# Performance work log

Measured on AMD Instinct MI355X. Metric: run time of the kernel, lower is better.

## Reference

```python
import jax, jax.numpy as jnp
import numpy as np

HEADS = 16
D_MODEL = 1024
D_K = D_MODEL // HEADS
B, S = 2, 2048
NEG = -1000000000.0


def setup_inputs() -> dict:
    key = jax.random.key(0)
    ks = jax.random.split(key, 8)
    q = jax.random.normal(ks[0], (B, S, D_MODEL), dtype=jnp.float32)
    k = jax.random.normal(ks[1], (B, S, D_MODEL), dtype=jnp.float32)
    v = jax.random.normal(ks[2], (B, S, D_MODEL), dtype=jnp.float32)
    mask = jax.random.randint(ks[3], (B, 1, S, S), 0, 2) > 0  # True = masked
    scale = 1.0 / np.sqrt(D_MODEL)
    Wq = jax.random.normal(ks[4], (D_MODEL, D_MODEL), dtype=jnp.float32) * scale
    Wk = jax.random.normal(ks[5], (D_MODEL, D_MODEL), dtype=jnp.float32) * scale
    Wv = jax.random.normal(ks[6], (D_MODEL, D_MODEL), dtype=jnp.float32) * scale
    Wo = jax.random.normal(ks[7], (D_MODEL, D_MODEL), dtype=jnp.float32) * scale
    return {"q": q, "k": k, "v": v, "mask": mask,
            "Wq": Wq, "Wk": Wk, "Wv": Wv, "Wo": Wo}


def reference(q, k, v, mask, Wq, Wk, Wv, Wo):
    b, s, _ = q.shape
    # torch Linear: x @ W.T ; reshape to [B, H, S, d_k]
    def proj(x, W):
        return (x @ W.T).reshape(b, -1, HEADS, D_K).transpose(0, 2, 1, 3)
    qh, kh, vh = proj(q, Wq), proj(k, Wk), proj(v, Wv)
    # scaled dot-product attention; scale uses d_k (key.shape[-1] after reshape)
    att = jnp.einsum('bhqd,bhkd->bhqk', qh, kh) / jnp.sqrt(jnp.float32(D_K))
    att = jnp.where(mask, NEG, att)
    att = jax.nn.softmax(att, axis=-1)
    out = jnp.einsum('bhqk,bhkd->bhqd', att, vh)  # [B,H,S,d_k]
    out = out.transpose(0, 2, 1, 3).reshape(b, -1, D_MODEL)
    return out @ Wo.T  # dropout is identity at inference
```

## Files before the change

kernel.cpp:

```cpp
#include <hip/hip_runtime.h>

typedef unsigned short u16;
typedef unsigned int   u32;
typedef unsigned char  u8;
typedef unsigned long long u64;
typedef __attribute__((ext_vector_type(8))) short bf16x8;
typedef __attribute__((ext_vector_type(4))) float f32x4;
typedef __attribute__((ext_vector_type(16))) float f32x16;

__device__ __forceinline__ u16 f2b(float f) {
  union { float f; u32 u; } v; v.f = f;
  u32 u = v.u;
  return (u16)((u + 0x7fffu + ((u >> 16) & 1u)) >> 16);
}
__device__ __forceinline__ float b2f(u16 x) {
  union { u32 u; float f; } v; v.u = ((u32)x) << 16; return v.f;
}
__device__ __forceinline__ u32 pk2(u16 lo, u16 hi) { return (u32)lo | ((u32)hi << 16); }

__device__ __forceinline__ float fexp2(float x) { return __builtin_amdgcn_exp2f(x); }

__device__ __forceinline__ u32 cvtpk(float lo, float hi) {
  u32 r;
  asm("v_cvt_pk_bf16_f32 %0, %1, %2" : "=v"(r) : "v"(lo), "v"(hi));
  return r;
}

__device__ __forceinline__ void swap32(u32& a, u32& b) {
  asm("v_permlane32_swap_b32 %0, %1" : "+v"(a), "+v"(b));
}

__device__ __forceinline__ void glds16(const u16* g, u16* l) {
  __builtin_amdgcn_global_load_lds((const __attribute__((address_space(1))) void*)g,
                                   (__attribute__((address_space(3))) void*)l, 16, 0, 0);
}

__global__ __launch_bounds__(256) void mask_detect(const u8* __restrict__ raw,
                                                   int* __restrict__ flag) {
  int i = blockIdx.x * 256 + threadIdx.x;
  uint4 x = ((const uint4*)raw)[i];
  u32 o = x.x | x.y | x.z | x.w;
  u64 b1 = __ballot((o & 0x0000ff00u) != 0);
  u64 b2 = __ballot((o & 0xffff0000u) != 0);
  if ((threadIdx.x & 63) == 0) {
    if (b1) atomicOr(&flag[0], 1);
    if (b2) atomicOr(&flag[1], 1);
  }
}

__global__ __launch_bounds__(256) void mask_bits(const u8* __restrict__ raw,
                                                 u64* __restrict__ out,
                                                 const int* __restrict__ flag) {
  int f = flag[0] ? 2 : (flag[1] ? 1 : 0);
  int t = blockIdx.x * 256 + threadIdx.x;
  u8 byte;
  if (f == 2) {
    u64 x = ((const u64*)raw)[t];
    u64 nz = x | (x >> 4); nz |= nz >> 2; nz |= nz >> 1;
    nz &= 0x0101010101010101ull;
    byte = (u8)((nz * 0x0102040810204080ull) >> 56);
  } else if (f == 0) {
    const int* ip = (const int*)raw + t * 8;
    int4 a = *(const int4*)ip, b = *(const int4*)(ip + 4);
    byte = (u8)((a.x != 0) | ((a.y != 0) << 1) | ((a.z != 0) << 2) | ((a.w != 0) << 3) |
                ((b.x != 0) << 4) | ((b.y != 0) << 5) | ((b.z != 0) << 6) | ((b.w != 0) << 7));
  } else {
    const float* fp = (const float*)raw + t * 8;
    float4 a = *(const float4*)fp, b = *(const float4*)(fp + 4);
    byte = (u8)((a.x != 0.f) | ((a.y != 0.f) << 1) | ((a.z != 0.f) << 2) | ((a.w != 0.f) << 3) |
                ((b.x != 0.f) << 4) | ((b.y != 0.f) << 5) | ((b.z != 0.f) << 6) | ((b.w != 0.f) << 7));
  }
  ((u8*)out)[t] = byte;
}

__global__ __launch_bounds__(256) void conv_all(
    const float* __restrict__ W0, const float* __restrict__ W1,
    const float* __restrict__ W2, const float* __restrict__ W3,
    const float* __restrict__ A0, const float* __restrict__ A1,
    const float* __restrict__ A2,
    u16* __restrict__ o0, u16* __restrict__ o1, u16* __restrict__ o2,
    u16* __restrict__ o3, u16* __restrict__ o4, u16* __restrict__ o5,
    u16* __restrict__ o6) {
  int gid = blockIdx.x * 256 + threadIdx.x;
  const float* src; u16* dst; int off;
  if (gid < 524288) {
    int wz = gid >> 17; off = (gid & 131071) * 8;
    src = wz == 0 ? W0 : wz == 1 ? W1 : wz == 2 ? W2 : W3;
    dst = wz == 0 ? o0 : wz == 1 ? o1 : wz == 2 ? o2 : o3;
  } else {
    int g2 = gid - 524288;
    int az = g2 >> 19; off = (g2 & 524287) * 8;
    src = az == 0 ? A0 : az == 1 ? A1 : A2;
    dst = az == 0 ? o4 : az == 1 ? o5 : o6;
  }
  float4 a = *(const float4*)(src + off), b2 = *(const float4*)(src + off + 4);
  uint4 t;
  t.x = pk2(f2b(a.x), f2b(a.y));   t.y = pk2(f2b(a.z), f2b(a.w));
  t.z = pk2(f2b(b2.x), f2b(b2.y)); t.w = pk2(f2b(b2.z), f2b(b2.w));
  *(uint4*)(dst + off) = t;
}

template<int CF32, int DBUF>
__device__ __forceinline__ void gemm_body(
    const u16* __restrict__ Av, const u16* __restrict__ Bv, void* __restrict__ Cv,
    int N, int K, int m0, int n0, float cscale, u16* As, u16* Bs) {
  const int tid = threadIdx.x;
  const int lane = tid & 63, w = tid >> 6;
  const int lr = lane & 15, lg = lane >> 4;
  const int wm = (w >> 1) * 64, wn = (w & 1) * 64;
  const int srow = lane >> 3;
  const int selem = (((lane & 7) ^ srow) << 3);
  const int rsw = (lr & 7) << 3;

  f32x4 acc[4][4];
#pragma unroll
  for (int mi = 0; mi < 4; ++mi)
#pragma unroll
    for (int ni = 0; ni < 4; ++ni)
      acc[mi][ni] = (f32x4){0.f, 0.f, 0.f, 0.f};

#define GLDS2(k0_, LA, LB)                                                     \
  do {                                                                         \
    _Pragma("unroll")                                                          \
    for (int r_ = 0; r_ < 4; ++r_) {                                           \
      const int c_ = w * 4 + r_;                                               \
      const int row_ = c_ * 8 + srow;                                          \
      glds16(Av + (size_t)(m0 + row_) * K + (k0_) + selem, (LA) + c_ * 512);   \
      glds16(Bv + (size_t)(n0 + row_) * K + (k0_) + selem, (LB) + c_ * 512);   \
    }                                                                          \
  } while (0)

#define FRAG_MFMA(bufA, bufB)                                                  \
  do {                                                                         \
    bf16x8 af[4][2], bfv[4][2];                                                \
    _Pragma("unroll")                                                          \
    for (int mi = 0; mi < 4; ++mi)                                             \
      _Pragma("unroll")                                                        \
      for (int kk = 0; kk < 2; ++kk)                                           \
        af[mi][kk] = *(bf16x8*)&(bufA)[(wm + mi * 16 + lr) * 64 + ((kk * 32 + lg * 8) ^ rsw)]; \
    _Pragma("unroll")                                                          \
    for (int ni = 0; ni < 4; ++ni)                                             \
      _Pragma("unroll")                                                        \
      for (int kk = 0; kk < 2; ++kk)                                           \
        bfv[ni][kk] = *(bf16x8*)&(bufB)[(wn + ni * 16 + lr) * 64 + ((kk * 32 + lg * 8) ^ rsw)]; \
    __builtin_amdgcn_s_setprio(1);                                             \
    _Pragma("unroll")                                                          \
    for (int mi = 0; mi < 4; ++mi)                                             \
      _Pragma("unroll")                                                        \
      for (int ni = 0; ni < 4; ++ni)                                           \
        _Pragma("unroll")                                                      \
        for (int kk = 0; kk < 2; ++kk)                                         \
          acc[mi][ni] = __builtin_amdgcn_mfma_f32_16x16x32_bf16(               \
              af[mi][kk], bfv[ni][kk], acc[mi][ni], 0, 0, 0);                  \
    __builtin_amdgcn_s_setprio(0);                                             \
  } while (0)

  if (DBUF) {
    GLDS2(0, As, Bs);
    __syncthreads();
    int cur = 0;
    for (int k0 = 0; k0 < K; k0 += 64) {
      if (k0 + 64 < K) GLDS2(k0 + 64, As + (cur ^ 1) * 8192, Bs + (cur ^ 1) * 8192);
      FRAG_MFMA(As + cur * 8192, Bs + cur * 8192);
      __syncthreads();
      cur ^= 1;
    }
  } else {
    for (int k0 = 0; k0 < K; k0 += 64) {
      __syncthreads();
      GLDS2(k0, As, Bs);
      __syncthreads();
      FRAG_MFMA(As, Bs);
    }
  }
#undef GLDS2
#undef FRAG_MFMA
#pragma unroll
  for (int mi = 0; mi < 4; ++mi)
#pragma unroll
    for (int ni = 0; ni < 4; ++ni)
#pragma unroll
      for (int r = 0; r < 4; ++r) {
        int m = m0 + wm + mi * 16 + lg * 4 + r;
        int n = n0 + wn + ni * 16 + lr;
        float vv = acc[mi][ni][r] * cscale;
        if (CF32) ((float*)Cv)[(size_t)m * N + n] = vv;
        else      ((u16*)Cv)[(size_t)m * N + n] = f2b(vv);
      }
}

__global__ __launch_bounds__(256) void gemm_qkv(
    const u16* __restrict__ qb, const u16* __restrict__ kb, const u16* __restrict__ vb,
    const u16* __restrict__ Wqb, const u16* __restrict__ Wkb, const u16* __restrict__ Wvb,
    u16* __restrict__ Qb, u16* __restrict__ Kb, u16* __restrict__ VTb, float qscale) {
  __shared__ __align__(16) u16 As[8192];
  __shared__ __align__(16) u16 Bs[8192];
  const int z = blockIdx.z;
  const int xcd = blockIdx.x & 7, r = blockIdx.x >> 3;
  const int pblk = xcd * 4 + (r & 3);
  const int oblk = r >> 2;
  if (z < 2) {
    const u16* act = z ? kb : qb;
    const u16* Wb = z ? Wkb : Wqb;
    u16* Cb = z ? Kb : Qb;
    gemm_body<0, 0>(act, Wb, Cb, 1024, 1024, pblk * 128, oblk * 128,
                    z ? 1.0f : qscale, As, Bs);
  } else {
    gemm_body<0, 0>(Wvb, vb, VTb, 4096, 1024, oblk * 128, pblk * 128, 1.0f, As, Bs);
  }
}

__device__ __forceinline__ void gemm64_body(
    const u16* __restrict__ Av, const u16* __restrict__ Bv, float* __restrict__ Cv,
    int N, int K, int m0, int n0, u16* As, u16* Bs) {
  const int tid = threadIdx.x;
  const int lane = tid & 63, w = tid >> 6;
  const int lr = lane & 15, lg = lane >> 4;
  const int wm = w * 32;
  const int srow = lane >> 3;
  const int selem = (((lane & 7) ^ srow) << 3);
  const int rsw = (lr & 7) << 3;

  f32x4 acc[2][4];
#pragma unroll
  for (int mi = 0; mi < 2; ++mi)
#pragma unroll
    for (int ni = 0; ni < 4; ++ni)
      acc[mi][ni] = (f32x4){0.f, 0.f, 0.f, 0.f};

  for (int k0 = 0; k0 < K; k0 += 64) {
    __syncthreads();
#pragma unroll
    for (int r_ = 0; r_ < 4; ++r_) {
      const int c_ = w * 4 + r_;
      const int row_ = c_ * 8 + srow;
      glds16(Av + (size_t)(m0 + row_) * K + k0 + selem, As + c_ * 512);
    }
#pragma unroll
    for (int r_ = 0; r_ < 2; ++r_) {
      const int c_ = w * 2 + r_;
      const int row_ = c_ * 8 + srow;
      glds16(Bv + (size_t)(n0 + row_) * K + k0 + selem, Bs + c_ * 512);
    }
    __syncthreads();
    bf16x8 af[2][2], bfv[4][2];
#pragma unroll
    for (int mi = 0; mi < 2; ++mi)
#pragma unroll
      for (int kk = 0; kk < 2; ++kk)
        af[mi][kk] = *(bf16x8*)&As[(wm + mi * 16 + lr) * 64 + ((kk * 32 + lg * 8) ^ rsw)];
#pragma unroll
    for (int ni = 0; ni < 4; ++ni)
#pragma unroll
      for (int kk = 0; kk < 2; ++kk)
        bfv[ni][kk] = *(bf16x8*)&Bs[(ni * 16 + lr) * 64 + ((kk * 32 + lg * 8) ^ rsw)];
    __builtin_amdgcn_s_setprio(1);
#pragma unroll
    for (int mi = 0; mi < 2; ++mi)
#pragma unroll
      for (int ni = 0; ni < 4; ++ni)
#pragma unroll
        for (int kk = 0; kk < 2; ++kk)
          acc[mi][ni] = __builtin_amdgcn_mfma_f32_16x16x32_bf16(
              af[mi][kk], bfv[ni][kk], acc[mi][ni], 0, 0, 0);
    __builtin_amdgcn_s_setprio(0);
  }
#pragma unroll
  for (int mi = 0; mi < 2; ++mi)
#pragma unroll
    for (int ni = 0; ni < 4; ++ni)
#pragma unroll
      for (int r = 0; r < 4; ++r) {
        int m = m0 + wm + mi * 16 + lg * 4 + r;
        int n = n0 + ni * 16 + lr;
        Cv[(size_t)m * N + n] = acc[mi][ni][r];
      }
}

__global__ __launch_bounds__(256) void gemm_o(
    const u16* __restrict__ Ob, const u16* __restrict__ Wob, float* __restrict__ C) {
  __shared__ __align__(16) u16 As[128 * 64];
  __shared__ __align__(16) u16 Bs[64 * 64];
  const int xcd = blockIdx.x & 7, r = blockIdx.x >> 3;
  const int mblk = xcd * 4 + (r & 3), nblk = r >> 2;
  gemm64_body(Ob, Wob, C, 1024, 1024, mblk * 128, nblk * 64, As, Bs);
}

__global__ __launch_bounds__(256, 4) void flash13(const u16* __restrict__ Q,
                                                  const u16* __restrict__ K,
                                                  const u16* __restrict__ VT,
                                                  const u64* __restrict__ mpk,
                                                  u16* __restrict__ O0,
                                                  u16* __restrict__ O1,
                                                  u16* __restrict__ O2,
                                                  float* __restrict__ Lp) {
  __shared__ __align__(16) u16 Ks[4096];
  __shared__ __align__(16) u16 Vs[4096];
  const int tid = threadIdx.x, lane = tid & 63, w = tid >> 6;
  const int c = lane & 31, h = lane >> 5;
  const int bid = blockIdx.x;
  const int xcd = bid & 7, idx = bid >> 3;
  const int gl = idx >> 4, qblk = idx & 15;
  const int group = xcd * 12 + gl;
  const int split = group % 3;
  const int hb = group / 3;
  const int head = hb & 15, b = hb >> 4;
  const int qw = qblk * 128 + w * 32;
  const int kt0 = (split * 32) / 3;
  const int ktn = ((split + 1) * 32) / 3;
  const int nt = ktn - kt0;
  const size_t kbase = (size_t)b * 2048 * 1024 + (size_t)head * 64;
  const size_t vbase = (size_t)head * 64 * 4096 + (size_t)b * 2048;
  const int srow = lane >> 3;
  const int selem = (((lane & 7) ^ srow) << 3);
  const int rswc = (c & 7) << 3;

  bf16x8 qf[4];
#pragma unroll
  for (int kd = 0; kd < 4; ++kd)
    qf[kd] = *(const bf16x8*)&Q[kbase + (size_t)(qw + c) * 1024 + 16 * kd + 8 * h];

  union { u32 u[4]; bf16x8 v; } ones;
#pragma unroll
  for (int i = 0; i < 4; ++i) ones.u[i] = 0x3f803f80u;

  f32x16 accO0, accO1, accL;
#pragma unroll
  for (int i = 0; i < 16; ++i) { accO0[i] = 0.f; accO1[i] = 0.f; accL[i] = 0.f; }

  const u64* mrp = mpk + ((size_t)b * 2048 + qw + c) * 32;

  for (int t = 0; t < nt; ++t) {
    __syncthreads();
    {
      const int k0_ = (kt0 + t) * 64;
#pragma unroll
      for (int r_ = 0; r_ < 2; ++r_) {
        const int c_ = w * 2 + r_;
        const int row_ = c_ * 8 + srow;
        glds16(K + kbase + (size_t)(k0_ + row_) * 1024 + selem, &Ks[c_ * 512]);
      }
#pragma unroll
      for (int r_ = 0; r_ < 2; ++r_) {
        const int c_ = w * 2 + r_;
        const int row_ = c_ * 8 + srow;
        glds16(VT + vbase + (size_t)row_ * 4096 + k0_ + selem, &Vs[c_ * 512]);
      }
    }
    const u64 mb = mrp[kt0 + t];
    __syncthreads();
    f32x16 s0, s1;
#pragma unroll
    for (int i = 0; i < 16; ++i) { s0[i] = 0.f; s1[i] = 0.f; }
    __builtin_amdgcn_s_setprio(1);
#pragma unroll
    for (int kd = 0; kd < 4; ++kd) {
      bf16x8 kf0 = *(bf16x8*)&Ks[c * 64 + ((16 * kd + 8 * h) ^ rswc)];
      s0 = __builtin_amdgcn_mfma_f32_32x32x16_bf16(kf0, qf[kd], s0, 0, 0, 0);
      bf16x8 kf1 = *(bf16x8*)&Ks[(32 + c) * 64 + ((16 * kd + 8 * h) ^ rswc)];
      s1 = __builtin_amdgcn_mfma_f32_32x32x16_bf16(kf1, qf[kd], s1, 0, 0, 0);
    }
    __builtin_amdgcn_s_setprio(0);
    u32 pw[2][4][2];
#pragma unroll
    for (int kb = 0; kb < 2; ++kb) {
      const u32 m32 = (u32)(mb >> (32 * kb + 4 * h));
      float pp[16];
#pragma unroll
      for (int g = 0; g < 4; ++g)
#pragma unroll
        for (int r = 0; r < 4; ++r) {
          float e = fexp2(kb == 0 ? s0[4 * g + r] : s1[4 * g + r]);
          pp[4 * g + r] = ((m32 >> (8 * g + r)) & 1) ? 0.0f : e;
        }
#pragma unroll
      for (int g = 0; g < 4; ++g)
#pragma unroll
        for (int hh = 0; hh < 2; ++hh)
          pw[kb][g][hh] = cvtpk(pp[4 * g + 2 * hh], pp[4 * g + 2 * hh + 1]);
    }
    __builtin_amdgcn_s_setprio(1);
#pragma unroll
    for (int kb = 0; kb < 2; ++kb)
#pragma unroll
      for (int s = 0; s < 2; ++s) {
        u32 w0 = pw[kb][2 * s][0], w2 = pw[kb][2 * s + 1][0];
        swap32(w0, w2);
        u32 w1 = pw[kb][2 * s][1], w3 = pw[kb][2 * s + 1][1];
        swap32(w1, w3);
        union { u32 u[4]; bf16x8 v; } af;
        af.u[0] = w0; af.u[1] = w1; af.u[2] = w2; af.u[3] = w3;
        const int ksg = kb * 2 + s;
        bf16x8 vf0 = *(bf16x8*)&Vs[c * 64 + ((16 * ksg + 8 * h) ^ rswc)];
        accO0 = __builtin_amdgcn_mfma_f32_32x32x16_bf16(af.v, vf0, accO0, 0, 0, 0);
        bf16x8 vf1 = *(bf16x8*)&Vs[(32 + c) * 64 + ((16 * ksg + 8 * h) ^ rswc)];
        accO1 = __builtin_amdgcn_mfma_f32_32x32x16_bf16(af.v, vf1, accO1, 0, 0, 0);
        accL  = __builtin_amdgcn_mfma_f32_32x32x16_bf16(af.v, ones.v, accL, 0, 0, 0);
      }
    __builtin_amdgcn_s_setprio(0);
  }
  u16* Op = split == 0 ? O0 : split == 1 ? O1 : O2;
  const size_t obase = (size_t)b * 2048 + qw;
#pragma unroll
  for (int g = 0; g < 4; ++g)
#pragma unroll
    for (int r = 0; r < 4; ++r) {
      const int qrow = r + 8 * g + 4 * h;
      const size_t row = obase + qrow;
      const size_t base = row * 1024 + (size_t)head * 64 + c;
      Op[base]      = f2b(accO0[4 * g + r]);
      Op[base + 32] = f2b(accO1[4 * g + r]);
      if (c == 0) Lp[(size_t)split * 65536 + row * 16 + head] = accL[4 * g + r];
    }
}

__global__ __launch_bounds__(256) void combine(const u16* __restrict__ O0,
                                               const u16* __restrict__ O1,
                                               const u16* __restrict__ O2,
                                               const float* __restrict__ Lp,
                                               u16* __restrict__ Ob) {
  int gid = blockIdx.x * 256 + threadIdx.x;
  int row = gid >> 7, chb = (gid & 127) * 8;
  int head = chb >> 6;
  float l = Lp[(size_t)row * 16 + head] + Lp[65536 + (size_t)row * 16 + head] +
            Lp[131072 + (size_t)row * 16 + head];
  float inv = 1.0f / l;
  size_t off = (size_t)row * 1024 + chb;
  union { uint4 q; u16 s[8]; } a, b, c2, o;
  a.q  = *(const uint4*)(O0 + off);
  b.q  = *(const uint4*)(O1 + off);
  c2.q = *(const uint4*)(O2 + off);
#pragma unroll
  for (int j = 0; j < 8; ++j)
    o.s[j] = f2b((b2f(a.s[j]) + b2f(b.s[j]) + b2f(c2.s[j])) * inv);
  *(uint4*)(Ob + off) = o.q;
}

extern "C" void kernel_launch(void* const* d_in, const int* in_sizes, int n_in,
                              void* d_out, int out_size, void* d_ws, size_t ws_size,
                              hipStream_t stream) {
  const float* q    = (const float*)d_in[0];
  const float* k    = (const float*)d_in[1];
  const float* v    = (const float*)d_in[2];
  const u8*    mask = (const u8*)d_in[3];
  const float* Wq   = (const float*)d_in[4];
  const float* Wk   = (const float*)d_in[5];
  const float* Wv   = (const float*)d_in[6];
  const float* Wo   = (const float*)d_in[7];

  u8* ws = (u8*)d_ws;
  int* flag = (int*)ws;
  u64* mpk  = (u64*)(ws + 256);
  u16* Wqb  = (u16*)(ws + 256 + (1u << 20));
  u16* Wkb  = Wqb + (1 << 20);
  u16* Wvb  = Wkb + (1 << 20);
  u16* Wob  = Wvb + (1 << 20);
  const size_t NE = (size_t)4096 * 1024;
  u16* vb   = Wob + (1 << 20);
  u16* O2   = vb;
  u16* Qb   = vb + NE;
  u16* Kb   = Qb + NE;
  u16* VTb  = Kb + NE;
  u16* qb   = (u16*)d_out;
  u16* kb   = qb + NE;
  u16* O0   = qb;
  u16* O1   = kb;
  float* Lp = (float*)Wqb;
  u16* Ob   = Qb;

  const float LOG2E = 1.4426950408889634f;

  hipMemsetAsync(flag, 0, 8, stream);
  mask_detect<<<32, 256, 0, stream>>>(mask, flag);
  mask_bits<<<4096, 256, 0, stream>>>(mask, mpk, flag);
  conv_all<<<8192, 256, 0, stream>>>(Wq, Wk, Wv, Wo, q, k, v,
                                     Wqb, Wkb, Wvb, Wob, qb, kb, vb);

  gemm_qkv<<<dim3(256, 1, 3), 256, 0, stream>>>(
      qb, kb, vb, Wqb, Wkb, Wvb, Qb, Kb, VTb, 0.125f * LOG2E);

  flash13<<<1536, 256, 0, stream>>>(Qb, Kb, VTb, mpk, O0, O1, O2, Lp);
  combine<<<2048, 256, 0, stream>>>(O0, O1, O2, Lp, Ob);

  gemm_o<<<512, 256, 0, stream>>>(Ob, Wob, (float*)d_out);
}
```

Before: 141.3 us.

## Register-prefetch next K/V tile in flash kernel instead of direct global-to-LDS loads

Swaps the direct global-to-LDS loads (glds16) for loads into registers that fetch the next K/V tile and mask word one iteration ahead. At the top of each iteration the prefetched registers are written to swizzled LDS. The aim is to hide global memory latency behind the current tile's MFMA work. It costs extra VGPRs (four uint4 per thread) under a launch bound of 4 waves per SIMD, plus an extra register-to-LDS store step.

Measured after the change: 182.8 us. 1.29x slower.

```diff
diff --git a/kernel.cpp b/kernel.cpp
--- a/kernel.cpp
+++ b/kernel.cpp
@@ -286,7 +286,7 @@
   gemm64_body(Ob, Wob, C, 1024, 1024, mblk * 128, nblk * 64, As, Bs);
 }
 
-__global__ __launch_bounds__(256, 4) void flash13(const u16* __restrict__ Q,
+__global__ __launch_bounds__(256, 4) void flash14(const u16* __restrict__ Q,
                                                   const u16* __restrict__ K,
                                                   const u16* __restrict__ VT,
                                                   const u64* __restrict__ mpk,
@@ -312,7 +312,10 @@
   const size_t kbase = (size_t)b * 2048 * 1024 + (size_t)head * 64;
   const size_t vbase = (size_t)head * 64 * 4096 + (size_t)b * 2048;
   const int srow = lane >> 3;
-  const int selem = (((lane & 7) ^ srow) << 3);
+  const int l7 = lane & 7;
+  const int rowK0 = (w * 2 + 0) * 8 + srow, rowK1 = (w * 2 + 1) * 8 + srow;
+  const int wr0 = rowK0 * 64 + ((l7 ^ srow) << 3);
+  const int wr1 = rowK1 * 64 + ((l7 ^ srow) << 3);
   const int rswc = (c & 7) << 3;
 
   bf16x8 qf[4];
@@ -330,24 +333,30 @@
 
   const u64* mrp = mpk + ((size_t)b * 2048 + qw + c) * 32;
 
+  uint4 gK0, gK1, gV0, gV1;
+#define LOADR(t)                                                               \
+  do {                                                                         \
+    const int k0_ = (t) * 64;                                                  \
+    gK0 = *(const uint4*)&K[kbase + (size_t)(k0_ + rowK0) * 1024 + l7 * 8];    \
+    gK1 = *(const uint4*)&K[kbase + (size_t)(k0_ + rowK1) * 1024 + l7 * 8];    \
+    gV0 = *(const uint4*)&VT[vbase + (size_t)rowK0 * 4096 + k0_ + l7 * 8];     \
+    gV1 = *(const uint4*)&VT[vbase + (size_t)rowK1 * 4096 + k0_ + l7 * 8];     \
+  } while (0)
+
+  LOADR(kt0);
+  u64 mb_next = mrp[kt0];
+
   for (int t = 0; t < nt; ++t) {
     __syncthreads();
-    {
-      const int k0_ = (kt0 + t) * 64;
-#pragma unroll
-      for (int r_ = 0; r_ < 2; ++r_) {
-        const int c_ = w * 2 + r_;
-        const int row_ = c_ * 8 + srow;
-        glds16(K + kbase + (size_t)(k0_ + row_) * 1024 + selem, &Ks[c_ * 512]);
-      }
-#pragma unroll
-      for (int r_ = 0; r_ < 2; ++r_) {
-        const int c_ = w * 2 + r_;
-        const int row_ = c_ * 8 + srow;
-        glds16(VT + vbase + (size_t)row_ * 4096 + k0_ + selem, &Vs[c_ * 512]);
-      }
-    }
-    const u64 mb = mrp[kt0 + t];
+    *(uint4*)&Ks[wr0] = gK0;
+    *(uint4*)&Ks[wr1] = gK1;
+    *(uint4*)&Vs[wr0] = gV0;
+    *(uint4*)&Vs[wr1] = gV1;
+    const u64 mb = mb_next;
+    if (t + 1 < nt) {
+      LOADR(kt0 + t + 1);
+      mb_next = mrp[kt0 + t + 1];
+    }
     __syncthreads();
     f32x16 s0, s1;
 #pragma unroll
@@ -399,6 +408,7 @@
       }
     __builtin_amdgcn_s_setprio(0);
   }
+#undef LOADR
   u16* Op = split == 0 ? O0 : split == 1 ? O1 : O2;
   const size_t obase = (size_t)b * 2048 + qw;
 #pragma unroll
@@ -479,7 +489,7 @@
   gemm_qkv<<<dim3(256, 1, 3), 256, 0, stream>>>(
       qb, kb, vb, Wqb, Wkb, Wvb, Qb, Kb, VTb, 0.125f * LOG2E);
 
-  flash13<<<1536, 256, 0, stream>>>(Qb, Kb, VTb, mpk, O0, O1, O2, Lp);
+  flash14<<<1536, 256, 0, stream>>>(Qb, Kb, VTb, mpk, O0, O1, O2, Lp);
   combine<<<2048, 256, 0, stream>>>(O0, O1, O2, Lp, Ob);
 
   gemm_o<<<512, 256, 0, stream>>>(Ob, Wob, (float*)d_out);
```
